# Kernel optimization log

Measured on AMD Instinct MI355X. Metric: run time of the kernel, lower is better.

Reference implementation:

```python
import jax, jax.numpy as jnp
import numpy as np

SG_SLOPE = 20.0  # fast_sigmoid surrogate slope
THRESHOLD = 1.0

@jax.custom_vjp
def spike_fn(v):
    # Heaviside spike with fast-sigmoid surrogate gradient
    return (v > 0).astype(v.dtype)

def _spike_fwd(v):
    return spike_fn(v), v

def _spike_bwd(v, g):
    return (g / (SG_SLOPE * jnp.abs(v) + 1.0) ** 2,)

spike_fn.defvjp(_spike_fwd, _spike_bwd)

def setup_inputs() -> dict:
    key = jax.random.key(0)
    T, IN, H, HEADS, O = 8192, 192, 1024, 5, 2
    dt = 0.004
    sp = float(np.log1p(np.exp(0.5413)))  # softplus(param) ~= 1.0
    tau_syn_h, tau_mem_h = 0.01 * sp, 0.02 * sp
    tau_syn_r = np.array([0.01, 0.02, 0.05, 0.1, 0.2]) * sp
    tau_mem_r = np.array([0.02, 0.05, 0.1, 0.2, 0.5]) * sp
    k1, k2, k3, k4 = jax.random.split(key, 4)
    x = jax.random.normal(k1, (T, IN), jnp.float32)
    W_in = jax.random.normal(k2, (H, IN), jnp.float32) / np.sqrt(IN)
    V = jax.random.normal(k3, (H, H), jnp.float32) / np.sqrt(H)
    b_rec = jnp.zeros((H,), jnp.float32)
    W_out = jax.random.normal(k4, (HEADS, O, H), jnp.float32) / np.sqrt(H)
    return {
        "x": x, "W_in": W_in, "V": V, "b_rec": b_rec, "W_out": W_out,
        "alpha_h": jnp.float32(np.exp(-dt / tau_syn_h)),
        "beta_h": jnp.float32(np.exp(-dt / tau_mem_h)),
        "alpha_r": jnp.asarray(np.exp(-dt / tau_syn_r), jnp.float32),
        "beta_r": jnp.asarray(np.exp(-dt / tau_mem_r), jnp.float32),
    }

def reference(x, W_in, V, b_rec, W_out, alpha_h, beta_h, alpha_r, beta_r):
    H = W_in.shape[0]
    HEADS, O, _ = W_out.shape
    dt_f32 = x.dtype

    def step(carry, x_t):
        inp_prev, spk, syn_h, mem_h, syn_r, mem_r = carry
        # hidden RSynaptic (note: fc_hidden consumes the PREVIOUS input, one-step delay)
        cur = W_in @ inp_prev + V @ spk + b_rec
        syn_h_new = alpha_h * syn_h + cur
        reset = jax.lax.stop_gradient(spk)  # zero-reset uses previous spike, detached
        mem_h_new = (beta_h * mem_h + syn_h_new) * (1.0 - reset)
        spk_new = spike_fn(mem_h_new - THRESHOLD)
        # readout heads consume the PREVIOUS hidden spike (pre-update)
        r_in = jnp.einsum("hoc,c->ho", W_out, spk)  # [HEADS, 2]
        syn_r_new = alpha_r[:, None] * syn_r + r_in
        mem_r_new = beta_r[:, None] * mem_r + syn_r_new  # reset_mechanism='none'
        out = mem_r_new.mean(axis=0)  # average over readout heads
        return (x_t, spk_new, syn_h_new, mem_h_new, syn_r_new, mem_r_new), out

    init = (
        jnp.zeros_like(x[0]),
        jnp.zeros((H,), dt_f32),
        jnp.zeros((H,), dt_f32),
        jnp.zeros((H,), dt_f32),
        jnp.zeros((HEADS, O), dt_f32),
        jnp.zeros((HEADS, O), dt_f32),
    )
    _, preds = jax.lax.scan(step, init, x)
    return preds  # [T, 2]
```

## Files before the change

kernel.cpp:

```cpp
#include <hip/hip_runtime.h>
#include <hip/hip_bf16.h>


constexpr int T_STEPS = 8192;
constexpr int IN_DIM  = 192;
constexpr int H_DIM   = 1024;
constexpr int NBLK    = 32;
constexpr int RING    = 4;

__global__ void k_clear(unsigned int* __restrict__ p, int n) {
    int i = blockIdx.x * blockDim.x + threadIdx.x;
    if (i < n) p[i] = 0u;
}

__global__ __launch_bounds__(576, 1) void k_phase1(
    const float* __restrict__ x,
    const float* __restrict__ W_in,
    const float* __restrict__ V,
    const float* __restrict__ b_rec,
    const float* __restrict__ alpha_h_p,
    const float* __restrict__ beta_h_p,
    unsigned long long* __restrict__ ringFlags,
    uint2* __restrict__ raster)
{
    const int tid   = threadIdx.x;
    const int blk   = blockIdx.x;
    const int w     = tid >> 6;
    const int l     = tid & 63;
    const bool syncw = (w == 8);
    const int r_local = l >> 4;
    const int cg      = l & 15;
    const int row   = (blk << 5) + (w << 2) + r_local;

    __shared__ unsigned int       bits_lds[2][NBLK];
    __shared__ unsigned long long combine[2];

    if (tid < NBLK) { bits_lds[0][tid] = 0u; bits_lds[1][tid] = 0u; }
    if (tid == 0)   { combine[0] = 0ull; combine[1] = 0ull; }

    float4 vfrag[16];
    float  wfrag[12];
    float  b_r = 0.f;
    if (!syncw) {
        const float4* vp = (const float4*)(V + (size_t)row * H_DIM + cg * 64);
        #pragma unroll
        for (int i = 0; i < 16; ++i) vfrag[i] = vp[i];
        const float* wp = W_in + row * IN_DIM + cg * 12;
        #pragma unroll
        for (int i = 0; i < 12; ++i) wfrag[i] = wp[i];
        b_r = b_rec[row];
    }
    const float ah = alpha_h_p[0];
    const float bh = beta_h_p[0];

    const float* xptr = x + cg * 12;
    float xr[12];
    #pragma unroll
    for (int i = 0; i < 12; ++i) xr[i] = 0.0f;

    float syn = 0.f, mem = 0.f, prev = 0.f;

    __syncthreads();

    for (int t = 0; t < T_STEPS; ++t) {
        const int rs = (t + 1) & 1;
        const int wsl = t & 1;

        if (!syncw) {
            const float4* xp4 = (const float4*)xptr;
            float4 f0 = xp4[0], f1 = xp4[1], f2 = xp4[2];

            unsigned int b0 = bits_lds[rs][2 * cg];
            unsigned int b1 = bits_lds[rs][2 * cg + 1];

            float a0 = 0.f, a1 = 0.f;
            #pragma unroll
            for (int i = 0; i < 8; ++i) {
                a0 = fmaf((float)((b0 >> (4 * i + 0)) & 1u), vfrag[i].x, a0);
                a0 = fmaf((float)((b0 >> (4 * i + 1)) & 1u), vfrag[i].y, a0);
                a0 = fmaf((float)((b0 >> (4 * i + 2)) & 1u), vfrag[i].z, a0);
                a0 = fmaf((float)((b0 >> (4 * i + 3)) & 1u), vfrag[i].w, a0);
                a1 = fmaf((float)((b1 >> (4 * i + 0)) & 1u), vfrag[8 + i].x, a1);
                a1 = fmaf((float)((b1 >> (4 * i + 1)) & 1u), vfrag[8 + i].y, a1);
                a1 = fmaf((float)((b1 >> (4 * i + 2)) & 1u), vfrag[8 + i].z, a1);
                a1 = fmaf((float)((b1 >> (4 * i + 3)) & 1u), vfrag[8 + i].w, a1);
            }
            #pragma unroll
            for (int i = 0; i < 12; ++i) a0 = fmaf(wfrag[i], xr[i], a0);
            float acc = a0 + a1;

            #pragma unroll
            for (int m = 1; m < 16; m <<= 1) acc += __shfl_xor(acc, m, 64);

            float cur = acc + b_r;
            syn = fmaf(ah, syn, cur);
            mem = fmaf(bh, mem, syn) * (1.0f - prev);
            float spk = (mem > 1.0f) ? 1.0f : 0.0f;
            prev = spk;

            unsigned long long bal = __ballot(spk > 0.5f);
            if (l == 0) {
                unsigned int nib = (unsigned int)(bal & 1ull)
                                 | ((unsigned int)((bal >> 16) & 1ull) << 1)
                                 | ((unsigned int)((bal >> 32) & 1ull) << 2)
                                 | ((unsigned int)((bal >> 48) & 1ull) << 3);
                unsigned long long add =
                    (1ull << 32) | ((unsigned long long)nib << (4 * w));
                unsigned long long old = __hip_atomic_fetch_add(&combine[wsl], add,
                        __ATOMIC_RELAXED, __HIP_MEMORY_SCOPE_WORKGROUP);
                unsigned long long nv = old + add;
                if ((nv >> 32) == 8ull) {
                    unsigned int bits = (unsigned int)nv;
                    unsigned int want = (unsigned int)(t + 1);
                    unsigned int w0 = (want << 16) | (bits & 0xffffu);
                    unsigned int w1 = (want << 16) | (bits >> 16);
                    unsigned long long pack =
                        (unsigned long long)w0 | ((unsigned long long)w1 << 32);
                    __hip_atomic_store(
                        &ringFlags[(size_t)(((t & (RING - 1)) << 5) | blk) << 3],
                        pack, __ATOMIC_RELAXED, __HIP_MEMORY_SCOPE_AGENT);
                    raster[(size_t)t * NBLK + blk] = make_uint2(w0, w1);
                    bits_lds[wsl][blk] = bits;
                    combine[wsl] = 0ull;
                }
            }

            #pragma unroll
            for (int i = 0; i < 4; ++i) {
                xr[i]     = (&f0.x)[i];
                xr[4 + i] = (&f1.x)[i];
                xr[8 + i] = (&f2.x)[i];
            }
            xptr += IN_DIM;
        } else {
            if (t + 1 < T_STEPS) {
                const bool act = (l < NBLK) && (l != blk);
                const unsigned int want = (unsigned int)(t + 1);
                const unsigned long long good =
                    ((unsigned long long)want << 16) |
                    ((unsigned long long)want << 48);
                const unsigned long long* p =
                    &ringFlags[(size_t)(((t & (RING - 1)) << 5) | l) << 3];
                unsigned long long vv = act
                    ? __hip_atomic_load(p, __ATOMIC_RELAXED, __HIP_MEMORY_SCOPE_AGENT)
                    : good;
                bool ok = (((vv >> 16) & 0xffffull) == want) && ((vv >> 48) == want);
                while (__any(!ok)) {
                    if (!ok) {
                        vv = __hip_atomic_load(p, __ATOMIC_RELAXED,
                                               __HIP_MEMORY_SCOPE_AGENT);
                        ok = (((vv >> 16) & 0xffffull) == want) && ((vv >> 48) == want);
                    }
                }
                if (act)
                    bits_lds[wsl][l] = (unsigned int)(vv & 0xffffull)
                                     | ((unsigned int)((vv >> 32) & 0xffffull) << 16);
            }
        }

        asm volatile("s_waitcnt lgkmcnt(0)" ::: "memory");
        __builtin_amdgcn_s_barrier();
        __builtin_amdgcn_sched_barrier(0);
    }
}

__global__ __launch_bounds__(256, 1) void k_readout_mm(
    const uint2* __restrict__ raster,
    const float* __restrict__ W_out,
    float* __restrict__ R)
{
    __shared__ float wlds[10 * 1033];
    for (int i = threadIdx.x; i < 10 * 1024; i += 256) {
        int r = i >> 10, c = i & 1023;
        wlds[r * 1033 + c] = W_out[i];
    }
    __syncthreads();

    int tid = threadIdx.x;
    if (tid >= 250) return;
    int tl = tid / 10, rowr = tid - tl * 10;
    int t = blockIdx.x * 25 + tl;
    if (t >= T_STEPS) return;

    float acc = 0.f;
    if (t > 0) {
        const uint2* wp = raster + (size_t)(t - 1) * NBLK;
        const float* wr = &wlds[rowr * 1033];
        for (int ww = 0; ww < NBLK; ++ww) {
            uint2 v = wp[ww];
            unsigned int bits = (v.x & 0xffffu) | ((v.y & 0xffffu) << 16);
            const float* wb = wr + ww * 32;
            #pragma unroll
            for (int j = 0; j < 32; ++j)
                acc = fmaf((float)((bits >> j) & 1u), wb[j], acc);
        }
    }
    R[t * 10 + rowr] = acc;
}

__global__ void k_scan(const float* __restrict__ R,
                       const float* __restrict__ alpha_r,
                       const float* __restrict__ beta_r,
                       float* __restrict__ memr_all)
{
    int lane = threadIdx.x;
    bool act = lane < 10;
    float a = act ? alpha_r[lane >> 1] : 0.f;
    float b = act ? beta_r[lane >> 1] : 0.f;
    float syn = 0.f, mem = 0.f;
    constexpr int PF = 8;
    float buf[PF];
    #pragma unroll
    for (int i = 0; i < PF; ++i) buf[i] = act ? R[i * 10 + lane] : 0.f;

    for (int tb = 0; tb < T_STEPS; tb += PF) {
        #pragma unroll
        for (int i = 0; i < PF; ++i) {
            int t = tb + i;
            syn = fmaf(a, syn, buf[i]);
            mem = fmaf(b, mem, syn);
            if (act) memr_all[t * 10 + lane] = mem;
            int tn = t + PF;
            buf[i] = (act && tn < T_STEPS) ? R[tn * 10 + lane] : 0.f;
        }
    }
}

__global__ void k_mean(const float* __restrict__ memr_all, float* __restrict__ out) {
    int g = blockIdx.x * blockDim.x + threadIdx.x;
    if (g >= T_STEPS * 2) return;
    int t = g >> 1, o = g & 1;
    const float* m = memr_all + t * 10 + o;
    out[g] = 0.2f * (m[0] + m[2] + m[4] + m[6] + m[8]);
}

extern "C" void kernel_launch(void* const* d_in, const int* in_sizes, int n_in,
                              void* d_out, int out_size, void* d_ws, size_t ws_size,
                              hipStream_t stream) {
    (void)in_sizes; (void)n_in; (void)out_size; (void)ws_size;
    const float* x       = (const float*)d_in[0];
    const float* W_in    = (const float*)d_in[1];
    const float* V       = (const float*)d_in[2];
    const float* b_rec   = (const float*)d_in[3];
    const float* W_out   = (const float*)d_in[4];
    const float* alpha_h = (const float*)d_in[5];
    const float* beta_h  = (const float*)d_in[6];
    const float* alpha_r = (const float*)d_in[7];
    const float* beta_r  = (const float*)d_in[8];
    float* out = (float*)d_out;

    char* wsb = (char*)d_ws;
    unsigned long long* ringFlags = (unsigned long long*)wsb;
    uint2* raster  = (uint2*)(wsb + RING * NBLK * 64);
    float* Rbuf    = (float*)(wsb + RING * NBLK * 64
                              + (size_t)T_STEPS * NBLK * 8);
    float* memr_all = Rbuf + (size_t)T_STEPS * 10;

    int nclr = RING * NBLK * 16;
    k_clear<<<(nclr + 255) / 256, 256, 0, stream>>>((unsigned int*)ringFlags, nclr);
    k_phase1<<<NBLK, 576, 0, stream>>>(x, W_in, V, b_rec, alpha_h, beta_h,
                                       ringFlags, raster);
    k_readout_mm<<<(T_STEPS + 24) / 25, 256, 0, stream>>>(raster, W_out, Rbuf);
    k_scan<<<1, 64, 0, stream>>>(Rbuf, alpha_r, beta_r, memr_all);
    k_mean<<<(T_STEPS * 2 + 255) / 256, 256, 0, stream>>>(memr_all, out);
}
```

Measured before the change: 18.47 ms.

## Replace shared ring flags with per-receiver mailboxes pushed by each producer

Each block's finishing wave now writes its spike bits and step tag into a private mailbox slot per destination block, instead of into one flag slot that all 31 consumers poll. Each block's sync wave then polls a contiguous row of mailboxes addressed to it. The goal is to cut contention and cross-CU traffic on heavily shared cache lines during the per-step grid synchronization. In exchange the producer issues 31 stores per step and the workspace grows, and the mailbox entries are no longer padded to separate cache lines.

Result: slower. 19.12 ms (+3.5%).

```diff
diff --git a/kernel.cpp b/kernel.cpp
--- a/kernel.cpp
+++ b/kernel.cpp
@@ -20,7 +20,7 @@
     const float* __restrict__ b_rec,
     const float* __restrict__ alpha_h_p,
     const float* __restrict__ beta_h_p,
-    unsigned long long* __restrict__ ringFlags,
+    unsigned long long* __restrict__ mbox,
     uint2* __restrict__ raster)
 {
     const int tid   = threadIdx.x;
@@ -63,7 +63,7 @@
     __syncthreads();
 
     for (int t = 0; t < T_STEPS; ++t) {
-        const int rs = (t + 1) & 1;
+        const int rs  = (t + 1) & 1;
         const int wsl = t & 1;
 
         if (!syncw) {
@@ -99,6 +99,7 @@
             prev = spk;
 
             unsigned long long bal = __ballot(spk > 0.5f);
+            unsigned int isLast = 0u, bitsAll = 0u;
             if (l == 0) {
                 unsigned int nib = (unsigned int)(bal & 1ull)
                                  | ((unsigned int)((bal >> 16) & 1ull) << 1)
@@ -109,16 +110,22 @@
                 unsigned long long old = __hip_atomic_fetch_add(&combine[wsl], add,
                         __ATOMIC_RELAXED, __HIP_MEMORY_SCOPE_WORKGROUP);
                 unsigned long long nv = old + add;
-                if ((nv >> 32) == 8ull) {
-                    unsigned int bits = (unsigned int)nv;
-                    unsigned int want = (unsigned int)(t + 1);
-                    unsigned int w0 = (want << 16) | (bits & 0xffffu);
-                    unsigned int w1 = (want << 16) | (bits >> 16);
-                    unsigned long long pack =
-                        (unsigned long long)w0 | ((unsigned long long)w1 << 32);
+                if ((nv >> 32) == 8ull) { isLast = 1u; bitsAll = (unsigned int)nv; }
+            }
+            isLast = __shfl(isLast, 0, 64);
+            if (isLast) {
+                unsigned int bits = __shfl(bitsAll, 0, 64);
+                unsigned int want = (unsigned int)(t + 1);
+                unsigned int w0 = (want << 16) | (bits & 0xffffu);
+                unsigned int w1 = (want << 16) | (bits >> 16);
+                unsigned long long pack =
+                    (unsigned long long)w0 | ((unsigned long long)w1 << 32);
+                if (l < NBLK && l != blk) {
                     __hip_atomic_store(
-                        &ringFlags[(size_t)(((t & (RING - 1)) << 5) | blk) << 3],
+                        &mbox[(size_t)(((t & (RING - 1)) * NBLK + l) * NBLK + blk)],
                         pack, __ATOMIC_RELAXED, __HIP_MEMORY_SCOPE_AGENT);
+                }
+                if (l == 0) {
                     raster[(size_t)t * NBLK + blk] = make_uint2(w0, w1);
                     bits_lds[wsl][blk] = bits;
                     combine[wsl] = 0ull;
@@ -136,15 +143,15 @@
             if (t + 1 < T_STEPS) {
                 const bool act = (l < NBLK) && (l != blk);
                 const unsigned int want = (unsigned int)(t + 1);
-                const unsigned long long good =
-                    ((unsigned long long)want << 16) |
-                    ((unsigned long long)want << 48);
                 const unsigned long long* p =
-                    &ringFlags[(size_t)(((t & (RING - 1)) << 5) | l) << 3];
-                unsigned long long vv = act
-                    ? __hip_atomic_load(p, __ATOMIC_RELAXED, __HIP_MEMORY_SCOPE_AGENT)
-                    : good;
-                bool ok = (((vv >> 16) & 0xffffull) == want) && ((vv >> 48) == want);
+                    &mbox[(size_t)(((t & (RING - 1)) * NBLK + blk) * NBLK + l)];
+                unsigned long long vv = 0ull;
+                bool ok = !act;
+                if (act) {
+                    vv = __hip_atomic_load(p, __ATOMIC_RELAXED,
+                                           __HIP_MEMORY_SCOPE_AGENT);
+                    ok = (((vv >> 16) & 0xffffull) == want) && ((vv >> 48) == want);
+                }
                 while (__any(!ok)) {
                     if (!ok) {
                         vv = __hip_atomic_load(p, __ATOMIC_RELAXED,
@@ -250,16 +257,16 @@
     float* out = (float*)d_out;
 
     char* wsb = (char*)d_ws;
-    unsigned long long* ringFlags = (unsigned long long*)wsb;
-    uint2* raster  = (uint2*)(wsb + RING * NBLK * 64);
-    float* Rbuf    = (float*)(wsb + RING * NBLK * 64
+    unsigned long long* mbox = (unsigned long long*)wsb;
+    uint2* raster  = (uint2*)(wsb + RING * NBLK * NBLK * 8);
+    float* Rbuf    = (float*)(wsb + RING * NBLK * NBLK * 8
                               + (size_t)T_STEPS * NBLK * 8);
     float* memr_all = Rbuf + (size_t)T_STEPS * 10;
 
-    int nclr = RING * NBLK * 16;
-    k_clear<<<(nclr + 255) / 256, 256, 0, stream>>>((unsigned int*)ringFlags, nclr);
+    int nclr = RING * NBLK * NBLK * 2;
+    k_clear<<<(nclr + 255) / 256, 256, 0, stream>>>((unsigned int*)mbox, nclr);
     k_phase1<<<NBLK, 576, 0, stream>>>(x, W_in, V, b_rec, alpha_h, beta_h,
-                                       ringFlags, raster);
+                                       mbox, raster);
     k_readout_mm<<<(T_STEPS + 24) / 25, 256, 0, stream>>>(raster, W_out, Rbuf);
     k_scan<<<1, 64, 0, stream>>>(Rbuf, alpha_r, beta_r, memr_all);
     k_mean<<<(T_STEPS * 2 + 255) / 256, 256, 0, stream>>>(memr_all, out);
```
